# Optimization experiments

Hardware: AMD Instinct MI355X
Metric: run time of the kernel (lower is better)

The kernel has to match this reference:

```python
import jax, jax.numpy as jnp
import numpy as np

B, T = 16, 512
S = T - 16  # sequence length after three 5x5 VALID convs and pool (H: T-4-4-4-5+1)
H = 64      # GRU hidden size


def setup_inputs() -> dict:
    key = jax.random.key(0)
    ks = jax.random.split(key, 20)
    def prm(k, shape, s=0.02):
        return jax.random.normal(k, shape, dtype=jnp.float32) * s
    return {
        "evaluation": jax.random.normal(ks[0], (B, 128, T), dtype=jnp.float32),
        "template":   jax.random.normal(ks[1], (B, 128, T), dtype=jnp.float32),
        "conv1_w": prm(ks[2], (16, 1, 5, 5), 0.05),  "conv1_b": prm(ks[3], (16,)),
        "conv2_w": prm(ks[4], (32, 16, 5, 5), 0.05), "conv2_b": prm(ks[5], (32,)),
        "conv3_w": prm(ks[6], (64, 32, 5, 5), 0.05), "conv3_b": prm(ks[7], (64,)),
        "lin1_w": prm(ks[8], (64, 3712)), "lin1_b": prm(ks[9], (64,)),
        "W_ih": prm(ks[10], (192, 64), 0.1), "W_hh": prm(ks[11], (192, 64), 0.1),
        "b_ih": prm(ks[12], (192,)),          "b_hh": prm(ks[13], (192,)),
        "att_w": prm(ks[14], (1, 64)),  "att_b": prm(ks[15], (1,)),
        "lin3_w": prm(ks[16], (128, 64)), "lin3_b": prm(ks[17], (128,)),
        "cls_w": prm(ks[18], (2, 128)),   "cls_b": prm(ks[19], (2,)),
    }


def _conv(x, w, b):
    # x: (N, C, H, W), w: (O, C, kh, kw), VALID, stride 1
    y = jax.lax.conv_general_dilated(x, w, (1, 1), 'VALID',
                                     dimension_numbers=('NCHW', 'OIHW', 'NCHW'))
    return y + b[None, :, None, None]


def _gru_seq(x, W_ih, W_hh, b_ih, b_hh):
    # x: (L, 64). One hidden state carried over the whole length (this mirrors
    # the torch module threading h0/h1 across samples in its Python loop).
    gi = x @ W_ih.T + b_ih  # (L, 192) input gates precomputed
    def step(h, gi_t):
        gh = W_hh @ h + b_hh
        r = jax.nn.sigmoid(gi_t[:H] + gh[:H])
        z = jax.nn.sigmoid(gi_t[H:2 * H] + gh[H:2 * H])
        n = jnp.tanh(gi_t[2 * H:] + r * gh[2 * H:])
        h_new = (1.0 - z) * n + z * h
        return h_new, h_new
    _, hs = jax.lax.scan(step, jnp.zeros((H,), x.dtype), gi)
    return hs  # (L, 64)


def reference(evaluation, template, conv1_w, conv1_b, conv2_w, conv2_b,
              conv3_w, conv3_b, lin1_w, lin1_b, W_ih, W_hh, b_ih, b_hh,
              att_w, att_b, lin3_w, lin3_b, cls_w, cls_b):
    # Shared conv trunk on stacked eval+template batch
    x = jnp.concatenate([evaluation, template], axis=0)      # (2B, 128, T)
    x = jnp.transpose(x, (0, 2, 1))[:, None]                 # (2B, 1, T, 128)
    x = _conv(x, conv1_w, conv1_b)                           # (2B, 16, T-4, 124)
    x = _conv(x, conv2_w, conv2_b)                           # (2B, 32, T-8, 120)
    x = _conv(x, conv3_w, conv3_b)                           # (2B, 64, T-12, 116)
    x = jax.lax.reduce_window(x, -jnp.inf, jax.lax.max,
                              (1, 1, 5, 2), (1, 1, 1, 2), 'VALID')  # (2B, 64, S, 58)
    # torch does a raw per-sample reshape (64, S, 58) -> (S, 3712)
    x = x.reshape(2 * B, S, 3712)
    x = x @ lin1_w.T + lin1_b                                # (2B, S, 64)
    # GRU: hidden carried across the batch -> one long scan per branch
    E = _gru_seq(x[:B].reshape(B * S, H), W_ih, W_hh, b_ih, b_hh).reshape(B, S, H)
    Tm = _gru_seq(x[B:].reshape(B * S, H), W_ih, W_hh, b_ih, b_hh).reshape(B, S, H)
    # alignment_weights[m, n] = <E[m], Tm[n]>, softmax over m (dim=0 per sample)
    A = jax.nn.softmax(jnp.einsum('bmd,bnd->bmn', E, Tm), axis=1)
    Tp = jnp.einsum('bmn,bnd->bmd', A, Tm)                   # template_prim
    dist = jnp.abs(Tp - E)                                    # (B, S, 64)
    att = jax.nn.softmax(jnp.einsum('bsd,d->bs', E, att_w[0]) + att_b[0], axis=1)
    rep = jnp.einsum('bs,bsd->bd', att, dist)                 # (B, 64)
    h = jax.nn.relu(rep)
    h = jax.nn.relu(h @ lin3_w.T + lin3_b)
    return h @ cls_w.T + cls_b                                # (B, 2)
```

## Files before the change

kernel.cpp:

```cpp
#include <hip/hip_runtime.h>
#include <hip/hip_bf16.h>
#include <math.h>


#define DEVI static __device__ __forceinline__
typedef __attribute__((ext_vector_type(8))) short short8;
typedef __attribute__((ext_vector_type(4))) float f32x4;
typedef __attribute__((ext_vector_type(8))) float f32x8;
typedef unsigned short ushort_t;

DEVI float fsig(float x)   { return 1.f / (1.f + __expf(-x)); }
DEVI float ftanh_(float x) { return 2.f / (1.f + __expf(-2.f * x)) - 1.f; }
DEVI float bf2f(ushort_t u) { union { unsigned int i; float f; } v; v.i = ((unsigned int)u) << 16; return v.f; }
DEVI ushort_t f2bf(float f) {
    union { float f; unsigned int i; } v; v.f = f;
    unsigned int r = v.i + 0x7FFF + ((v.i >> 16) & 1);
    return (ushort_t)(r >> 16);
}
DEVI f32x8 bf2f8(short8 s) {
    f32x8 r;
#pragma unroll
    for (int k = 0; k < 8; k++) r[k] = bf2f((ushort_t)s[k]);
    return r;
}
DEVI f32x8 max8(f32x8 a, f32x8 b) {
    f32x8 r;
#pragma unroll
    for (int k = 0; k < 8; k++) r[k] = fmaxf(a[k], b[k]);
    return r;
}

__global__ void pack_w2(const float* __restrict__ w2, ushort_t* __restrict__ w2p)
{
    for (int idx = blockIdx.x * 256 + threadIdx.x; idx < 15360; idx += gridDim.x * 256) {
        int kh = idx / 3072, rem = idx % 3072;
        int kw = rem / 512;
        int co = (rem >> 4) & 31, ci = rem & 15;
        float v = (kw < 5) ? w2[((co * 16 + ci) * 5 + kh) * 5 + kw] : 0.f;
        w2p[idx] = f2bf(v);
    }
}
__global__ void pack_w3(const float* __restrict__ w3, ushort_t* __restrict__ w3p)
{
    for (int idx = blockIdx.x * 256 + threadIdx.x; idx < 51200; idx += gridDim.x * 256) {
        int kh = idx / 10240, rem = idx % 10240;
        int kw = rem / 2048;
        int co = (rem >> 5) & 63, ci = rem & 31;
        w3p[idx] = f2bf(w3[((co * 32 + ci) * 5 + kh) * 5 + kw]);
    }
}
__global__ void pack_l1w(const float* __restrict__ l1w, ushort_t* __restrict__ l1wp)
{
    for (int idx = blockIdx.x * 256 + threadIdx.x; idx < 262144; idx += gridDim.x * 256) {
        int n = idx >> 12, kp = idx & 4095;
        int r = kp >> 6, j = kp & 63;
        float v = (j < 58) ? l1w[n * 3712 + r * 58 + j] : 0.f;
        l1wp[idx] = f2bf(v);
    }
}

__global__ void conv1_kernel(const float* __restrict__ ev,
                             const float* __restrict__ tmpl,
                             const float* __restrict__ wgt,
                             const float* __restrict__ bias,
                             ushort_t* __restrict__ out, int n0)
{
    const int h0  = blockIdx.x * 4;
    const int w0  = blockIdx.y * 62;
    const int nl  = blockIdx.z;
    const int n   = n0 + nl;
    const int tid = threadIdx.x;
    const int wl  = tid & 63;
    const int cg  = tid >> 6;
    const float* src = (n < 16) ? (ev + (size_t)n * 65536)
                                : (tmpl + (size_t)(n - 16) * 65536);

    __shared__ float tin[8 * 68];
    __shared__ float tw[16 * 25];

    float acc[4][4];
#pragma unroll
    for (int j = 0; j < 4; j++)
#pragma unroll
        for (int hh = 0; hh < 4; hh++) acc[j][hh] = 0.f;

    for (int idx = tid; idx < 528; idx += 256) {
        int cc = idx >> 3, r = idx & 7;
        tin[r * 68 + cc] = src[(w0 + cc) * 512 + h0 + r];
    }
    for (int idx = tid; idx < 400; idx += 256) tw[idx] = wgt[idx];
    __syncthreads();
#pragma unroll
    for (int kh = 0; kh < 5; kh++) {
#pragma unroll
        for (int kw = 0; kw < 5; kw++) {
            float iv[4];
#pragma unroll
            for (int hh = 0; hh < 4; hh++)
                iv[hh] = tin[(hh + kh) * 68 + wl + kw];
#pragma unroll
            for (int j = 0; j < 4; j++) {
                float wv = tw[(cg * 4 + j) * 25 + kh * 5 + kw];
#pragma unroll
                for (int hh = 0; hh < 4; hh++)
                    acc[j][hh] = fmaf(wv, iv[hh], acc[j][hh]);
            }
        }
    }
    if (wl < 62) {
#pragma unroll
        for (int hh = 0; hh < 4; hh++) {
            ushort_t pk[4];
#pragma unroll
            for (int j = 0; j < 4; j++)
                pk[j] = f2bf(acc[j][hh] + bias[cg * 4 + j]);
            ushort_t* dst = out + ((size_t)(nl * 508 + h0 + hh) * 124 + w0 + wl) * 16 + cg * 4;
            *(uint2*)dst = *(uint2*)pk;
        }
    }
}

template<int CI, int CO, int NF, int MF, int NHI, int W_T, int KSTEPS,
         int KW_TOT, int H_IN, int W_IN, bool PAD2, int MAXB>
__global__ __launch_bounds__(256, MAXB) void conv_mfma(
    const ushort_t* __restrict__ in, const ushort_t* __restrict__ wpk,
    const float* __restrict__ bias, ushort_t* __restrict__ out)
{
    constexpr int H_OUT = H_IN - 4;
    constexpr int W_OUT = W_IN - 4;
    constexpr int HALO  = W_T + 6;
    constexpr int OCT   = CI / 8;
    constexpr int AROWS = 4 * NHI + 4;
    constexpr int APL   = AROWS * HALO;
    constexpr int BPL   = KW_TOT * CO;

    const int h0 = blockIdx.x * (4 * NHI);
    const int w0 = blockIdx.y * W_T;
    const int nl = blockIdx.z;
    const int tid  = threadIdx.x;
    const int wv   = tid >> 6;
    const int lane = tid & 63;
    const int l16  = lane & 15;
    const int kq   = lane >> 4;

    __shared__ __align__(16) ushort_t As[OCT * APL * 8];
    __shared__ __align__(16) ushort_t Bs[OCT * BPL * 8];

    f32x4 acc[NHI][MF][NF];
#pragma unroll
    for (int hi = 0; hi < NHI; hi++)
#pragma unroll
        for (int mi = 0; mi < MF; mi++)
#pragma unroll
            for (int ni = 0; ni < NF; ni++)
                acc[hi][mi][ni] = f32x4{0.f, 0.f, 0.f, 0.f};

    for (int idx = tid; idx < OCT * APL; idx += 256) {
        int oct = idx / APL, e = idx - oct * APL;
        int r = e / HALO, c = e - r * HALO;
        const ushort_t* src = in + ((size_t)((nl * H_IN + h0 + r) * W_IN + w0 + c)) * CI + oct * 8;
        *(short8*)&As[idx * 8] = *(const short8*)src;
    }

    const int aoct = PAD2 ? (kq & 1) : kq;
    const int kwq  = PAD2 ? (kq >> 1) : 0;

#pragma unroll
    for (int kh = 0; kh < 5; kh++) {
        __syncthreads();
        for (int idx = tid; idx < OCT * BPL; idx += 256) {
            int oct = idx / BPL, e = idx - oct * BPL;
            int kw = e / CO, co = e - kw * CO;
            const ushort_t* src = wpk + ((size_t)((kh * KW_TOT + kw) * CO + co)) * CI + oct * 8;
            *(short8*)&Bs[idx * 8] = *(const short8*)src;
        }
        __syncthreads();
#pragma unroll
        for (int st = 0; st < KSTEPS; st++) {
            const int colq = (PAD2 ? st * 2 : st) + kwq;
            short8 bfv[NF];
#pragma unroll
            for (int ni = 0; ni < NF; ni++)
                bfv[ni] = *(const short8*)&Bs[(aoct * BPL + colq * CO + ni * 16 + l16) * 8];
#pragma unroll
            for (int hi = 0; hi < NHI; hi++) {
                short8 af[MF];
#pragma unroll
                for (int mi = 0; mi < MF; mi++)
                    af[mi] = *(const short8*)&As[(aoct * APL + (hi * 4 + wv + kh) * HALO + mi * 16 + l16 + colq) * 8];
#pragma unroll
                for (int mi = 0; mi < MF; mi++)
#pragma unroll
                    for (int ni = 0; ni < NF; ni++)
                        acc[hi][mi][ni] = __builtin_amdgcn_mfma_f32_16x16x32_bf16(
                            af[mi], bfv[ni], acc[hi][mi][ni], 0, 0, 0);
            }
        }
    }

#pragma unroll
    for (int hi = 0; hi < NHI; hi++) {
        const int h = h0 + hi * 4 + wv;
        if (h < H_OUT) {
#pragma unroll
            for (int mi = 0; mi < MF; mi++) {
#pragma unroll
                for (int ni = 0; ni < NF; ni++) {
                    int co = ni * 16 + l16;
                    float bv = bias[co];
#pragma unroll
                    for (int reg = 0; reg < 4; reg++) {
                        int w = w0 + mi * 16 + kq * 4 + reg;
                        if (w < W_OUT)
                            out[((size_t)(nl * H_OUT + h) * W_OUT + w) * CO + co] =
                                f2bf(acc[hi][mi][ni][reg] + bv);
                    }
                }
            }
        }
    }
}

__global__ __launch_bounds__(512) void pool_fused(const ushort_t* __restrict__ a3,
                                                  ushort_t* __restrict__ pooled)
{
    const int nl = blockIdx.y;
    const int s0 = blockIdx.x * 16;
    const int t  = threadIdx.x;
    __shared__ ushort_t L[4 * 3712];

    const int j = t >> 3, oct = t & 7;
    const ushort_t* base = a3 + (size_t)nl * 3712000 + (size_t)(2 * j) * 64 + oct * 8;
    ushort_t* dst = pooled + (size_t)nl * 1841152;

#define LOADROW(rr) max8(bf2f8(*(const short8*)(base + (size_t)(rr) * 7424)), \
                         bf2f8(*(const short8*)(base + (size_t)(rr) * 7424 + 64)))
    f32x8 w0, w1, w2v, w3v;
    if (t < 464) {
        w0  = LOADROW(s0);
        w1  = LOADROW(s0 + 1);
        w2v = LOADROW(s0 + 2);
        w3v = LOADROW(s0 + 3);
    }
    for (int g = 0; g < 4; g++) {
        if (t < 464) {
#pragma unroll
            for (int k = 0; k < 4; k++) {
                int s = s0 + g * 4 + k;
                f32x8 w4 = LOADROW(s + 4);
                f32x8 mx = max8(max8(max8(w0, w1), max8(w2v, w3v)), w4);
#pragma unroll
                for (int u = 0; u < 8; u++)
                    L[k * 3712 + (oct * 8 + u) * 58 + j] = f2bf(mx[u]);
                w0 = w1; w1 = w2v; w2v = w3v; w3v = w4;
            }
        }
        __syncthreads();
        const int sg = s0 + g * 4;
        for (int e = t; e < 14848; e += 512) {
            int k = e / 3712, r = e - k * 3712;
            int c = r / 58, jj = r - c * 58;
            dst[(size_t)c * 28768 + (sg + k) * 58 + jj] = L[e];
        }
        __syncthreads();
    }
#undef LOADROW
}

__global__ __launch_bounds__(256) void lin1_mfma(
    const ushort_t* __restrict__ pooled, const ushort_t* __restrict__ l1wp,
    float* __restrict__ xb, int n0, int RT)
{
    const int mt  = blockIdx.x;
    const int kqb = blockIdx.y;
    const int r0  = mt * 64;
    const int t   = threadIdx.x;
    const int wv  = t >> 6, lane = t & 63, l16 = lane & 15, kq = lane >> 4;

    __shared__ __align__(16) ushort_t As[8 * 64 * 8];
    __shared__ __align__(16) ushort_t Bs[8 * 64 * 8];

    f32x4 acc[4];
#pragma unroll
    for (int ni = 0; ni < 4; ni++) acc[ni] = f32x4{0.f, 0.f, 0.f, 0.f};

    for (int kb = 0; kb < 16; kb++) {
        const int k0 = kqb * 1024 + kb * 64;
        const int r  = k0 >> 6;
        __syncthreads();
        for (int idx = t; idx < 512; idx += 256) {
            int oct = idx >> 6, row = idx & 63;
            int rr = r0 + row;
            short8 v = short8{0, 0, 0, 0, 0, 0, 0, 0};
            if (rr < RT)
                v = *(const short8*)(pooled + (size_t)rr * 3712 + r * 58 + oct * 8);
            *(short8*)&As[idx * 8] = v;
        }
        for (int idx = t; idx < 512; idx += 256) {
            int oct = idx >> 6, co = idx & 63;
            *(short8*)&Bs[idx * 8] =
                *(const short8*)(l1wp + (size_t)co * 4096 + k0 + oct * 8);
        }
        __syncthreads();
#pragma unroll
        for (int st = 0; st < 2; st++) {
            short8 af = *(const short8*)&As[((st * 4 + kq) * 64 + wv * 16 + l16) * 8];
#pragma unroll
            for (int ni = 0; ni < 4; ni++) {
                short8 bfv = *(const short8*)&Bs[((st * 4 + kq) * 64 + ni * 16 + l16) * 8];
                acc[ni] = __builtin_amdgcn_mfma_f32_16x16x32_bf16(af, bfv, acc[ni], 0, 0, 0);
            }
        }
    }
#pragma unroll
    for (int ni = 0; ni < 4; ni++) {
        int co = ni * 16 + l16;
#pragma unroll
        for (int reg = 0; reg < 4; reg++) {
            int rr = r0 + wv * 16 + kq * 4 + reg;
            if (rr < RT)
                atomicAdd(&xb[((size_t)n0 * 496 + rr) * 64 + co], acc[ni][reg]);
        }
    }
}

__global__ __launch_bounds__(192) void gi_kernel(
    const float* __restrict__ x, const float* __restrict__ Wih,
    const float* __restrict__ bih, const float* __restrict__ l1b,
    float* __restrict__ gi)
{
    const int r0 = blockIdx.x * 64;
    const int j  = threadIdx.x;
    __shared__ float wls[192 * 65];
    __shared__ float xl[64 * 64];

    for (int idx = j; idx < 12288; idx += 192)
        wls[(idx >> 6) * 65 + (idx & 63)] = Wih[idx];
    for (int idx = j; idx < 4096; idx += 192)
        xl[idx] = x[(size_t)r0 * 64 + idx] + l1b[idx & 63];
    __syncthreads();

    float w[64];
#pragma unroll
    for (int d = 0; d < 64; d++) w[d] = wls[j * 65 + d];
    const float bj = bih[j];

    for (int s = 0; s < 64; s++) {
        float a = bj;
#pragma unroll
        for (int d = 0; d < 64; d++) a = fmaf(w[d], xl[s * 64 + d], a);
        gi[(size_t)(r0 + s) * 192 + j] = a;
    }
}

__global__ __launch_bounds__(64, 1) void gru_kernel(
    const float* __restrict__ gi, const float* __restrict__ Whh,
    const float* __restrict__ bhh, float* __restrict__ Eo,
    float* __restrict__ To)
{
    const int c  = blockIdx.x;
    const int br = c >> 8;
    const int q  = c & 255;
    const int i  = threadIdx.x;
    const float* gb = gi + (size_t)br * 7936 * 192;
    float* out = br ? To : Eo;

    float wr[64], wz[64], wn[64];
#pragma unroll
    for (int k = 0; k < 64; k++) wr[k] = Whh[i * 64 + k];
#pragma unroll
    for (int k = 0; k < 64; k++) wz[k] = Whh[(64 + i) * 64 + k];
#pragma unroll
    for (int k = 0; k < 64; k++) wn[k] = Whh[(128 + i) * 64 + k];
    const float bhr = bhh[i], bhz = bhh[64 + i], bhn = bhh[128 + i];

    __shared__ __align__(16) float hs[64];
    float h[64];
#pragma unroll
    for (int k = 0; k < 64; k++) h[k] = 0.f;
    float hown = 0.f;

    const int cs  = q * 31;
    int start = cs - 96;
    if (start < 0) start = 0;
    const int end = cs + 31;

    float pr[4], pz[4], pn[4];
#pragma unroll
    for (int u = 0; u < 4; u++) {
        int s = start + u;
        if (s < end) {
            const float* g = gb + (size_t)s * 192;
            pr[u] = g[i]; pz[u] = g[64 + i]; pn[u] = g[128 + i];
        } else { pr[u] = 0.f; pz[u] = 0.f; pn[u] = 0.f; }
    }

    int s = start;
    while (s < end) {
#pragma unroll
        for (int u = 0; u < 4; u++) {
            if (s < end) {
                float gr = pr[u], gz = pz[u], gn = pn[u];
                int sp = s + 4;
                if (sp < end) {
                    const float* g = gb + (size_t)sp * 192;
                    pr[u] = g[i]; pz[u] = g[64 + i]; pn[u] = g[128 + i];
                }
                float ar = bhr, az = bhz, an = bhn;
#pragma unroll
                for (int k = 0; k < 64; k++) {
                    ar = fmaf(wr[k], h[k], ar);
                    az = fmaf(wz[k], h[k], az);
                    an = fmaf(wn[k], h[k], an);
                }
                float r  = fsig(gr + ar);
                float z  = fsig(gz + az);
                float nv = ftanh_(gn + r * an);
                float hn = (1.f - z) * nv + z * hown;
                hown = hn;
                hs[i] = hn;
                __syncthreads();
#pragma unroll
                for (int k = 0; k < 16; k++) {
                    float4 v = ((const float4*)hs)[k];
                    h[4 * k + 0] = v.x; h[4 * k + 1] = v.y;
                    h[4 * k + 2] = v.z; h[4 * k + 3] = v.w;
                }
                __syncthreads();
                if (s >= cs) out[(size_t)s * 64 + i] = hn;
                s++;
            }
        }
    }
}

__global__ void scores_kernel(const float* __restrict__ E,
                              const float* __restrict__ Tm,
                              float* __restrict__ S)
{
    const int b  = blockIdx.z;
    const int m0 = blockIdx.y * 32;
    const int n0 = blockIdx.x * 64;
    const int t  = threadIdx.x;
    const int nl = t & 63, mg = t >> 6;
    __shared__ float El[32 * 64];
    __shared__ float Tms[64 * 65];

    for (int idx = t; idx < 2048; idx += 256) {
        int r = idx >> 6, d = idx & 63;
        int m = m0 + r;
        El[idx] = (m < 496) ? E[((size_t)b * 496 + m) * 64 + d] : 0.f;
    }
    for (int idx = t; idx < 4096; idx += 256) {
        int r = idx >> 6, d = idx & 63;
        int n = n0 + r;
        Tms[d * 65 + r] = (n < 496) ? Tm[((size_t)b * 496 + n) * 64 + d] : 0.f;
    }
    __syncthreads();

    float acc[8];
#pragma unroll
    for (int j = 0; j < 8; j++) acc[j] = 0.f;
#pragma unroll 4
    for (int d = 0; d < 64; d++) {
        float tv = Tms[d * 65 + nl];
#pragma unroll
        for (int j = 0; j < 8; j++)
            acc[j] = fmaf(El[(mg * 8 + j) * 64 + d], tv, acc[j]);
    }
    int n = n0 + nl;
    if (n < 496) {
#pragma unroll
        for (int j = 0; j < 8; j++) {
            int m = m0 + mg * 8 + j;
            if (m < 496) S[((size_t)b * 496 + m) * 496 + n] = acc[j];
        }
    }
}

__global__ void colsum_kernel(const float* __restrict__ S,
                              float* __restrict__ invZ)
{
    const int b  = blockIdx.y;
    const int n0 = blockIdx.x * 32;
    const int t  = threadIdx.x;
    const int c  = t & 31, rg = t >> 5;
    const int n  = n0 + c;
    float sum = 0.f;
    if (n < 496) {
        const float* base = S + (size_t)b * 246016 + n;
        for (int mm = rg * 62; mm < rg * 62 + 62; mm++)
            sum += __expf(base[(size_t)mm * 496]);
    }
    __shared__ float red[256];
    red[t] = sum;
    __syncthreads();
    if (t < 32) {
        float s = 0.f;
#pragma unroll
        for (int g = 0; g < 8; g++) s += red[g * 32 + t];
        if (n0 + t < 496) invZ[b * 496 + n0 + t] = 1.f / s;
    }
}

__global__ void tp_kernel(const float* __restrict__ S,
                          const float* __restrict__ Tm,
                          const float* __restrict__ invZ,
                          float* __restrict__ Tp)
{
    const int b  = blockIdx.y;
    const int m0 = blockIdx.x * 32;
    const int t  = threadIdx.x;
    const int d  = t & 63, mg = t >> 6;
    __shared__ float As2[32 * 128];
    __shared__ float Ts[128 * 64];
    float acc[8];
#pragma unroll
    for (int j = 0; j < 8; j++) acc[j] = 0.f;

    for (int nc = 0; nc < 512; nc += 128) {
        __syncthreads();
        for (int idx = t; idx < 4096; idx += 256) {
            int r = idx >> 7, cc = idx & 127;
            int m = m0 + r, n = nc + cc;
            As2[idx] = (m < 496 && n < 496)
                          ? __expf(S[((size_t)b * 496 + m) * 496 + n]) : 0.f;
        }
        for (int idx = t; idx < 8192; idx += 256) {
            int r = idx >> 6, dd = idx & 63;
            int n = nc + r;
            Ts[idx] = (n < 496)
                          ? Tm[((size_t)b * 496 + n) * 64 + dd] * invZ[b * 496 + n]
                          : 0.f;
        }
        __syncthreads();
#pragma unroll 4
        for (int nn = 0; nn < 128; nn++) {
            float tv = Ts[nn * 64 + d];
#pragma unroll
            for (int j = 0; j < 8; j++)
                acc[j] = fmaf(As2[(mg * 8 + j) * 128 + nn], tv, acc[j]);
        }
    }
#pragma unroll
    for (int j = 0; j < 8; j++) {
        int m = m0 + mg * 8 + j;
        if (m < 496) Tp[((size_t)b * 496 + m) * 64 + d] = acc[j];
    }
}

__global__ void attrep_kernel(const float* __restrict__ E,
                              const float* __restrict__ Tp,
                              const float* __restrict__ attw,
                              const float* __restrict__ attb,
                              float* __restrict__ rep)
{
    const int b = blockIdx.x;
    const int t = threadIdx.x;
    __shared__ float aw[64];
    __shared__ float lg[496];
    __shared__ float att[496];
    __shared__ float redm[4], reds[4];
    __shared__ float part[256];

    if (t < 64) aw[t] = attw[t];
    __syncthreads();
    for (int s = t; s < 496; s += 256) {
        const float* Er = E + ((size_t)b * 496 + s) * 64;
        float a = 0.f;
#pragma unroll
        for (int dd = 0; dd < 64; dd++) a = fmaf(Er[dd], aw[dd], a);
        lg[s] = a + attb[0];
    }
    __syncthreads();
    float m = -1e30f;
    for (int s = t; s < 496; s += 256) m = fmaxf(m, lg[s]);
    for (int off = 32; off > 0; off >>= 1)
        m = fmaxf(m, __shfl_xor(m, off, 64));
    if ((t & 63) == 0) redm[t >> 6] = m;
    __syncthreads();
    m = fmaxf(fmaxf(redm[0], redm[1]), fmaxf(redm[2], redm[3]));
    float sum = 0.f;
    for (int s = t; s < 496; s += 256) {
        float e = __expf(lg[s] - m);
        att[s] = e;
        sum += e;
    }
    for (int off = 32; off > 0; off >>= 1) sum += __shfl_xor(sum, off, 64);
    if ((t & 63) == 0) reds[t >> 6] = sum;
    __syncthreads();
    float inv = 1.f / (reds[0] + reds[1] + reds[2] + reds[3]);

    const int d = t & 63, sg = t >> 6;
    float p = 0.f;
    for (int k = 0; k < 124; k++) {
        int s = sg + 4 * k;
        size_t o = ((size_t)b * 496 + s) * 64 + d;
        p = fmaf(att[s] * inv, fabsf(Tp[o] - E[o]), p);
    }
    part[t] = p;
    __syncthreads();
    if (t < 64)
        rep[b * 64 + t] = part[t] + part[64 + t] + part[128 + t] + part[192 + t];
}

__global__ void mlp_kernel(const float* __restrict__ rep,
                           const float* __restrict__ W3,
                           const float* __restrict__ b3,
                           const float* __restrict__ Wc,
                           const float* __restrict__ bc,
                           float* __restrict__ out)
{
    const int b = blockIdx.x;
    const int t = threadIdx.x;
    __shared__ float hr[64];
    __shared__ float h2[128];
    if (t < 64) hr[t] = fmaxf(rep[b * 64 + t], 0.f);
    __syncthreads();
    float a = b3[t];
#pragma unroll
    for (int d = 0; d < 64; d++) a = fmaf(W3[t * 64 + d], hr[d], a);
    h2[t] = fmaxf(a, 0.f);
    __syncthreads();
    if (t < 2) {
        float o = bc[t];
        for (int k = 0; k < 128; k++) o = fmaf(Wc[t * 128 + k], h2[k], o);
        out[b * 2 + t] = o;
    }
}

extern "C" void kernel_launch(void* const* d_in, const int* in_sizes, int n_in,
                              void* d_out, int out_size, void* d_ws,
                              size_t ws_size, hipStream_t stream)
{
    const float* ev   = (const float*)d_in[0];
    const float* tmpl = (const float*)d_in[1];
    const float* w1   = (const float*)d_in[2];
    const float* b1   = (const float*)d_in[3];
    const float* w2   = (const float*)d_in[4];
    const float* b2   = (const float*)d_in[5];
    const float* w3   = (const float*)d_in[6];
    const float* b3   = (const float*)d_in[7];
    const float* l1w  = (const float*)d_in[8];
    const float* l1b  = (const float*)d_in[9];
    const float* wih  = (const float*)d_in[10];
    const float* whh  = (const float*)d_in[11];
    const float* bih  = (const float*)d_in[12];
    const float* bhh  = (const float*)d_in[13];
    const float* attw = (const float*)d_in[14];
    const float* attb = (const float*)d_in[15];
    const float* l3w  = (const float*)d_in[16];
    const float* l3b  = (const float*)d_in[17];
    const float* clw  = (const float*)d_in[18];
    const float* clb  = (const float*)d_in[19];

    float* ws = (float*)d_ws;
    float* xb    = ws;
    float* Eb    = xb + 1015808ull;
    float* Tb    = Eb + 507904ull;
    float* Tpb   = Tb + 507904ull;
    float* repb  = Tpb + 507904ull;
    float* w2pf  = repb + 1024ull;
    float* w3pf  = w2pf + 7680ull;
    float* l1wpf = w3pf + 25600ull;
    float* invZb = l1wpf + 131072ull;
    float* arena = invZb + 8192ull;
    const size_t PERSIST = 2713088ull;

    ushort_t* w2p  = (ushort_t*)w2pf;
    ushort_t* w3p  = (ushort_t*)w3pf;
    ushort_t* l1wp = (ushort_t*)l1wpf;

    const int cand[6] = {32, 16, 8, 4, 2, 1};
    int C = 0;
    for (int ci = 0; ci < 6; ci++) {
        size_t a = (size_t)cand[ci] * 2823680ull + 16384ull;
        if (a < 3936256ull) a = 3936256ull;
        if ((PERSIST + a) * sizeof(float) <= ws_size) { C = cand[ci]; break; }
    }
    if (C == 0) return;

    float*    S1 = arena;
    float*    S2 = arena + (size_t)C * 967680ull + 8192ull;
    float*    gib = arena;
    float*    Sb  = arena;

    ushort_t* a2  = (ushort_t*)S1;
    ushort_t* pooled = (ushort_t*)S1;
    ushort_t* a1  = (ushort_t*)S2;
    ushort_t* a3  = (ushort_t*)S2;

    hipMemsetAsync(xb, 0, 1015808ull * sizeof(float), stream);
    pack_w2<<<15, 256, 0, stream>>>(w2, w2p);
    pack_w3<<<50, 256, 0, stream>>>(w3, w3p);
    pack_l1w<<<256, 256, 0, stream>>>(l1w, l1wp);

    const int RT = C * 496;
    const int mtiles = (RT + 63) / 64;

    for (int n0 = 0; n0 < 32; n0 += C) {
        conv1_kernel<<<dim3(127, 2, C), 256, 0, stream>>>(ev, tmpl, w1, b1, a1, n0);
        conv_mfma<16, 32, 2, 4, 2, 64, 3, 6, 508, 124, true, 4>
            <<<dim3(63, 2, C), 256, 0, stream>>>(a1, w2p, b2, a2);
        conv_mfma<32, 64, 4, 2, 2, 32, 5, 5, 504, 120, false, 3>
            <<<dim3(63, 4, C), 256, 0, stream>>>(a2, w3p, b3, a3);
        pool_fused<<<dim3(31, C), 512, 0, stream>>>(a3, pooled);
        lin1_mfma<<<dim3(mtiles, 4), 256, 0, stream>>>(pooled, l1wp, xb, n0, RT);
    }

    gi_kernel<<<248, 192, 0, stream>>>(xb, wih, bih, l1b, gib);
    gru_kernel<<<512, 64, 0, stream>>>(gib, whh, bhh, Eb, Tb);

    scores_kernel<<<dim3(8, 16, 16), 256, 0, stream>>>(Eb, Tb, Sb);
    colsum_kernel<<<dim3(16, 16), 256, 0, stream>>>(Sb, invZb);
    tp_kernel<<<dim3(16, 16), 256, 0, stream>>>(Sb, Tb, invZb, Tpb);

    attrep_kernel<<<16, 256, 0, stream>>>(Eb, Tpb, attw, attb, repb);
    mlp_kernel<<<16, 128, 0, stream>>>(repb, l3w, l3b, clw, clb,
                                       (float*)d_out);
}
```

Measured before the change: 891.3 us.

## Enlarge conv1 row tiles and replace lin1 atomics with split-K partial buffers

```diff
diff --git a/kernel.cpp b/kernel.cpp
--- a/kernel.cpp
+++ b/kernel.cpp
@@ -59,13 +59,12 @@
     }
 }
 
-__global__ void conv1_kernel(const float* __restrict__ ev,
-                             const float* __restrict__ tmpl,
-                             const float* __restrict__ wgt,
-                             const float* __restrict__ bias,
-                             ushort_t* __restrict__ out, int n0)
-{
-    const int h0  = blockIdx.x * 4;
+__global__ __launch_bounds__(256) void conv1_kernel(
+    const float* __restrict__ ev, const float* __restrict__ tmpl,
+    const float* __restrict__ wgt, const float* __restrict__ bias,
+    ushort_t* __restrict__ out, int n0)
+{
+    const int h0  = blockIdx.x * 32;
     const int w0  = blockIdx.y * 62;
     const int nl  = blockIdx.z;
     const int n   = n0 + nl;
@@ -75,47 +74,53 @@
     const float* src = (n < 16) ? (ev + (size_t)n * 65536)
                                 : (tmpl + (size_t)(n - 16) * 65536);
 
-    __shared__ float tin[8 * 68];
-    __shared__ float tw[16 * 25];
-
-    float acc[4][4];
-#pragma unroll
-    for (int j = 0; j < 4; j++)
-#pragma unroll
-        for (int hh = 0; hh < 4; hh++) acc[j][hh] = 0.f;
-
-    for (int idx = tid; idx < 528; idx += 256) {
-        int cc = idx >> 3, r = idx & 7;
-        tin[r * 68 + cc] = src[(w0 + cc) * 512 + h0 + r];
+    __shared__ float tin[36 * 69];
+    __shared__ float tw[400];
+
+    for (int idx = tid; idx < 2376; idx += 256) {
+        int cc = idx / 36, r = idx - cc * 36;
+        int hh = h0 + r; if (hh > 511) hh = 511;
+        tin[r * 69 + cc] = src[(w0 + cc) * 512 + hh];
     }
     for (int idx = tid; idx < 400; idx += 256) tw[idx] = wgt[idx];
     __syncthreads();
-#pragma unroll
-    for (int kh = 0; kh < 5; kh++) {
-#pragma unroll
-        for (int kw = 0; kw < 5; kw++) {
-            float iv[4];
-#pragma unroll
-            for (int hh = 0; hh < 4; hh++)
-                iv[hh] = tin[(hh + kh) * 68 + wl + kw];
-#pragma unroll
-            for (int j = 0; j < 4; j++) {
-                float wv = tw[(cg * 4 + j) * 25 + kh * 5 + kw];
-#pragma unroll
-                for (int hh = 0; hh < 4; hh++)
-                    acc[j][hh] = fmaf(wv, iv[hh], acc[j][hh]);
+
+    for (int hg = 0; hg < 4; hg++) {
+        float acc[4][8];
+#pragma unroll
+        for (int j = 0; j < 4; j++)
+#pragma unroll
+            for (int hh = 0; hh < 8; hh++) acc[j][hh] = 0.f;
+#pragma unroll
+        for (int kh = 0; kh < 5; kh++) {
+#pragma unroll
+            for (int kw = 0; kw < 5; kw++) {
+                float iv[8];
+#pragma unroll
+                for (int hh = 0; hh < 8; hh++)
+                    iv[hh] = tin[(hg * 8 + hh + kh) * 69 + wl + kw];
+#pragma unroll
+                for (int j = 0; j < 4; j++) {
+                    float wv = tw[(cg * 4 + j) * 25 + kh * 5 + kw];
+#pragma unroll
+                    for (int hh = 0; hh < 8; hh++)
+                        acc[j][hh] = fmaf(wv, iv[hh], acc[j][hh]);
+                }
             }
         }
-    }
-    if (wl < 62) {
-#pragma unroll
-        for (int hh = 0; hh < 4; hh++) {
-            ushort_t pk[4];
-#pragma unroll
-            for (int j = 0; j < 4; j++)
-                pk[j] = f2bf(acc[j][hh] + bias[cg * 4 + j]);
-            ushort_t* dst = out + ((size_t)(nl * 508 + h0 + hh) * 124 + w0 + wl) * 16 + cg * 4;
-            *(uint2*)dst = *(uint2*)pk;
+        if (wl < 62) {
+#pragma unroll
+            for (int hh = 0; hh < 8; hh++) {
+                int h = h0 + hg * 8 + hh;
+                if (h < 508) {
+                    ushort_t pk[4];
+#pragma unroll
+                    for (int j = 0; j < 4; j++)
+                        pk[j] = f2bf(acc[j][hh] + bias[cg * 4 + j]);
+                    ushort_t* dst = out + ((size_t)(nl * 508 + h) * 124 + w0 + wl) * 16 + cg * 4;
+                    *(uint2*)dst = *(uint2*)pk;
+                }
+            }
         }
     }
 }
@@ -269,7 +274,7 @@
 
 __global__ __launch_bounds__(256) void lin1_mfma(
     const ushort_t* __restrict__ pooled, const ushort_t* __restrict__ l1wp,
-    float* __restrict__ xb, int n0, int RT)
+    float* __restrict__ xbp, int n0, int RT)
 {
     const int mt  = blockIdx.x;
     const int kqb = blockIdx.y;
@@ -312,6 +317,7 @@
             }
         }
     }
+    float* dst = xbp + (size_t)kqb * 1015808ull;
 #pragma unroll
     for (int ni = 0; ni < 4; ni++) {
         int co = ni * 16 + l16;
@@ -319,13 +325,13 @@
         for (int reg = 0; reg < 4; reg++) {
             int rr = r0 + wv * 16 + kq * 4 + reg;
             if (rr < RT)
-                atomicAdd(&xb[((size_t)n0 * 496 + rr) * 64 + co], acc[ni][reg]);
+                dst[((size_t)n0 * 496 + rr) * 64 + co] = acc[ni][reg];
         }
     }
 }
 
 __global__ __launch_bounds__(192) void gi_kernel(
-    const float* __restrict__ x, const float* __restrict__ Wih,
+    const float* __restrict__ xbp, const float* __restrict__ Wih,
     const float* __restrict__ bih, const float* __restrict__ l1b,
     float* __restrict__ gi)
 {
@@ -336,8 +342,11 @@
 
     for (int idx = j; idx < 12288; idx += 192)
         wls[(idx >> 6) * 65 + (idx & 63)] = Wih[idx];
-    for (int idx = j; idx < 4096; idx += 192)
-        xl[idx] = x[(size_t)r0 * 64 + idx] + l1b[idx & 63];
+    for (int idx = j; idx < 4096; idx += 192) {
+        size_t o = (size_t)r0 * 64 + idx;
+        xl[idx] = ((xbp[o] + xbp[1015808ull + o]) +
+                   (xbp[2031616ull + o] + xbp[3047424ull + o])) + l1b[idx & 63];
+    }
     __syncthreads();
 
     float w[64];
@@ -655,8 +664,8 @@
     const float* clb  = (const float*)d_in[19];
 
     float* ws = (float*)d_ws;
-    float* xb    = ws;
-    float* Eb    = xb + 1015808ull;
+    float* xbp   = ws;
+    float* Eb    = xbp + 4063232ull;
     float* Tb    = Eb + 507904ull;
     float* Tpb   = Tb + 507904ull;
     float* repb  = Tpb + 507904ull;
@@ -665,7 +674,7 @@
     float* l1wpf = w3pf + 25600ull;
     float* invZb = l1wpf + 131072ull;
     float* arena = invZb + 8192ull;
-    const size_t PERSIST = 2713088ull;
+    const size_t PERSIST = 5760512ull;
 
     ushort_t* w2p  = (ushort_t*)w2pf;
     ushort_t* w3p  = (ushort_t*)w3pf;
@@ -690,7 +699,6 @@
     ushort_t* a1  = (ushort_t*)S2;
     ushort_t* a3  = (ushort_t*)S2;
 
-    hipMemsetAsync(xb, 0, 1015808ull * sizeof(float), stream);
     pack_w2<<<15, 256, 0, stream>>>(w2, w2p);
     pack_w3<<<50, 256, 0, stream>>>(w3, w3p);
     pack_l1w<<<256, 256, 0, stream>>>(l1w, l1wp);
@@ -699,16 +707,16 @@
     const int mtiles = (RT + 63) / 64;
 
     for (int n0 = 0; n0 < 32; n0 += C) {
-        conv1_kernel<<<dim3(127, 2, C), 256, 0, stream>>>(ev, tmpl, w1, b1, a1, n0);
+        conv1_kernel<<<dim3(16, 2, C), 256, 0, stream>>>(ev, tmpl, w1, b1, a1, n0);
         conv_mfma<16, 32, 2, 4, 2, 64, 3, 6, 508, 124, true, 4>
             <<<dim3(63, 2, C), 256, 0, stream>>>(a1, w2p, b2, a2);
         conv_mfma<32, 64, 4, 2, 2, 32, 5, 5, 504, 120, false, 3>
             <<<dim3(63, 4, C), 256, 0, stream>>>(a2, w3p, b3, a3);
         pool_fused<<<dim3(31, C), 512, 0, stream>>>(a3, pooled);
-        lin1_mfma<<<dim3(mtiles, 4), 256, 0, stream>>>(pooled, l1wp, xb, n0, RT);
-    }
-
-    gi_kernel<<<248, 192, 0, stream>>>(xb, wih, bih, l1b, gib);
+        lin1_mfma<<<dim3(mtiles, 4), 256, 0, stream>>>(pooled, l1wp, xbp, n0, RT);
+    }
+
+    gi_kernel<<<248, 192, 0, stream>>>(xbp, wih, bih, l1b, gib);
     gru_kernel<<<512, 64, 0, stream>>>(gib, whh, bhh, Eb, Tb);
 
     scores_kernel<<<dim3(8, 16, 16), 256, 0, stream>>>(Eb, Tb, Sb);
```

New measurement: 956.4 us. 1.07x slower.
